# Kernel tuning notes

Hardware: AMD Instinct MI355X
Metric: run time of the kernel (lower is better)

Reference implementation:

```python
import jax, jax.numpy as jnp
import numpy as np

L, D, T, B = 4, 256, 4096, 8  # n_layer, hidden, seq_len, batch


def setup_inputs() -> dict:
    key = jax.random.key(0)
    ks = jax.random.split(key, 12)
    x = jax.random.normal(ks[0], (B, T, D), dtype=jnp.float32)
    # stable LRU diagonal init: |lambda| in [0.9, 0.999], phase in [0, pi/10]
    r = jax.random.uniform(ks[1], (L, D), minval=0.9, maxval=0.999)
    nu_log = jnp.log(-jnp.log(r))
    theta = jax.random.uniform(ks[2], (L, D), minval=1e-4, maxval=np.pi / 10)
    theta_log = jnp.log(theta)
    gamma_log = 0.5 * jnp.log(1.0 - r ** 2)  # normalization gamma = sqrt(1-|lam|^2)
    s = 0.02  # matches truncated_normal_init std
    B_re = s * jax.random.normal(ks[3], (L, D, D), dtype=jnp.float32)
    B_im = s * jax.random.normal(ks[4], (L, D, D), dtype=jnp.float32)
    C_re = s * jax.random.normal(ks[5], (L, D, D), dtype=jnp.float32)
    C_im = s * jax.random.normal(ks[6], (L, D, D), dtype=jnp.float32)
    D_vec = s * jax.random.normal(ks[7], (L, D), dtype=jnp.float32)
    Wg = s * jax.random.normal(ks[8], (L, D, D), dtype=jnp.float32)
    ln_scale = jnp.ones((L, D), dtype=jnp.float32)
    ln_bias = jnp.zeros((L, D), dtype=jnp.float32)
    return dict(x=x, nu_log=nu_log, theta_log=theta_log, gamma_log=gamma_log,
                B_re=B_re, B_im=B_im, C_re=C_re, C_im=C_im, D_vec=D_vec,
                Wg=Wg, ln_scale=ln_scale, ln_bias=ln_bias)


def _layer_norm(x, scale, bias):
    mu = x.mean(-1, keepdims=True)
    var = x.var(-1, keepdims=True)
    return (x - mu) / jnp.sqrt(var + 1e-5) * scale + bias


def _lru_scan(lam, bu):
    # lam: (D,) complex diagonal transition; bu: (T,B,D) complex inputs
    a = jnp.broadcast_to(lam, bu.shape)

    def comb(e1, e2):
        a1, b1 = e1
        a2, b2 = e2
        return a1 * a2, a2 * b1 + b2

    _, h = jax.lax.associative_scan(comb, (a, bu), axis=0)
    return h  # (T,B,D) complex


def reference(x, nu_log, theta_log, gamma_log, B_re, B_im, C_re, C_im, D_vec, Wg, ln_scale, ln_bias):
    u = jnp.transpose(x, (1, 0, 2))  # time-major (T,B,D), mirrors torch permute(1,0,2)
    for l in range(L):  # fixed small layer loop
        z = _layer_norm(u, ln_scale[l], ln_bias[l])
        lam = jnp.exp(-jnp.exp(nu_log[l]) + 1j * jnp.exp(theta_log[l]))  # (D,)
        Bm = B_re[l] + 1j * B_im[l]
        bu = jnp.einsum('tbd,ed->tbe', z.astype(jnp.complex64), Bm) * jnp.exp(gamma_log[l])
        h = _lru_scan(lam, bu)  # (T,B,D) complex state (h0 = 0, matching get_zero_internal_state)
        y = jnp.einsum('tbe,de->tbd', h, C_re[l] + 1j * C_im[l]).real + D_vec[l] * z
        y = y * jax.nn.sigmoid(jnp.einsum('tbd,ed->tbe', z, Wg[l]))  # gating=True output gate
        u = u + y  # residual
    return jnp.transpose(u, (1, 0, 2))  # back to (B,T,D)
```

## Files before the change

kernel.cpp:

```cpp
#include <hip/hip_runtime.h>
#include <hip/hip_bf16.h>

#define NLAYER 4
#define DDIM 256
#define TSEQ 4096
#define NBATCH 8
#define MROWS (NBATCH * TSEQ)
#define CLEN 32
#define NCHUNK (TSEQ / CLEN)

typedef float f32x4 __attribute__((ext_vector_type(4)));
typedef short bf16x8 __attribute__((ext_vector_type(8)));

__device__ __forceinline__ float bf2f(unsigned short u) {
    union { unsigned int i; float f; } v; v.i = ((unsigned int)u) << 16; return v.f;
}
__device__ __forceinline__ unsigned short f2bf(float f) {
    union { float f; unsigned int i; } v; v.f = f;
    unsigned int r = v.i + 0x7fffu + ((v.i >> 16) & 1u);
    return (unsigned short)(r >> 16);
}

__device__ __forceinline__ void gload16(const unsigned short* g, unsigned short* l) {
    __builtin_amdgcn_global_load_lds(
        (const __attribute__((address_space(1))) unsigned int*)g,
        (__attribute__((address_space(3))) unsigned int*)l, 16, 0, 0);
}

__global__ __launch_bounds__(256) void prepack_kernel(
    const float* __restrict__ nu_log, const float* __restrict__ theta_log,
    const float* __restrict__ gamma_log,
    const float* __restrict__ B_re, const float* __restrict__ B_im,
    const float* __restrict__ C_re, const float* __restrict__ C_im,
    const float* __restrict__ Wg,
    unsigned short* __restrict__ wBre, unsigned short* __restrict__ wBim,
    unsigned short* __restrict__ wWg, unsigned short* __restrict__ wCre,
    unsigned short* __restrict__ wCimn,
    float* __restrict__ lam_re, float* __restrict__ lam_im,
    float* __restrict__ lamC_re, float* __restrict__ lamC_im)
{
    int idx = blockIdx.x * 256 + threadIdx.x;
    const int total = NLAYER * DDIM * DDIM;
    if (idx < total) {
        int l = idx >> 16;
        int e = (idx >> 8) & 255;
        float gam = expf(gamma_log[l * DDIM + e]);
        wBre[idx]  = f2bf(B_re[idx] * gam);
        wBim[idx]  = f2bf(B_im[idx] * gam);
        wWg[idx]   = f2bf(Wg[idx]);
        wCre[idx]  = f2bf(C_re[idx]);
        wCimn[idx] = f2bf(-C_im[idx]);
    }
    if (idx < NLAYER * DDIM) {
        float mag = expf(-expf(nu_log[idx]));
        float th  = expf(theta_log[idx]);
        float ar = mag * cosf(th);
        float ai = mag * sinf(th);
        lam_re[idx] = ar;
        lam_im[idx] = ai;
        #pragma unroll
        for (int s = 0; s < 5; ++s) {
            float nr = ar * ar - ai * ai;
            float ni = 2.0f * ar * ai;
            ar = nr; ai = ni;
        }
        lamC_re[idx] = ar;
        lamC_im[idx] = ai;
    }
}

__global__ __launch_bounds__(256) void ln_kernel(
    const float* __restrict__ u, unsigned short* __restrict__ z,
    const float* __restrict__ scale, const float* __restrict__ bias,
    float2* __restrict__ rowStats)
{
    int wid = threadIdx.x >> 6;
    int lane = threadIdx.x & 63;
    int row = blockIdx.x * 4 + wid;
    const float4 v = *reinterpret_cast<const float4*>(u + (size_t)row * DDIM + lane * 4);
    float s  = v.x + v.y + v.z + v.w;
    float s2 = v.x * v.x + v.y * v.y + v.z * v.z + v.w * v.w;
    #pragma unroll
    for (int off = 32; off > 0; off >>= 1) {
        s  += __shfl_xor(s, off);
        s2 += __shfl_xor(s2, off);
    }
    float mu  = s * (1.0f / DDIM);
    float var = s2 * (1.0f / DDIM) - mu * mu;
    float inv = rsqrtf(var + 1e-5f);
    if (lane == 0) { float2 st; st.x = mu; st.y = inv; rowStats[row] = st; }
    float zv[4] = { v.x, v.y, v.z, v.w };
    ushort4 o;
    unsigned short* op = (unsigned short*)&o;
    #pragma unroll
    for (int j = 0; j < 4; ++j) {
        int d = lane * 4 + j;
        op[j] = f2bf((zv[j] - mu) * inv * scale[d] + bias[d]);
    }
    *reinterpret_cast<ushort4*>(z + (size_t)row * DDIM + lane * 4) = o;
}

__global__ __launch_bounds__(256) void gemm1_kernel(
    const unsigned short* __restrict__ z,
    const unsigned short* __restrict__ wBre, const unsigned short* __restrict__ wBim,
    const unsigned short* __restrict__ wWg,
    unsigned short* __restrict__ bure, unsigned short* __restrict__ buim,
    unsigned short* __restrict__ sg,
    const float* __restrict__ lam_re, const float* __restrict__ lam_im,
    float2* __restrict__ fin)
{
    const int m0 = blockIdx.x * 128;
    const int n0 = blockIdx.y * 64;

    __shared__ unsigned short Al[128 * 64];
    __shared__ unsigned short Wl[3][64 * 64];

    const int tid = threadIdx.x;
    const int lane = tid & 63;
    const int wid = tid >> 6;
    const int wr = wid >> 1, wc = wid & 1;
    const int lr = lane >> 3;
    const int lc = lane & 7;

    f32x4 acc[3][4][2] = {};

    for (int ko = 0; ko < 256; ko += 64) {
        #pragma unroll
        for (int it = 0; it < 4; ++it) {
            int s = wid * 4 + it;
            int r = s * 8 + lr;
            int gc = lc ^ (r & 7);
            gload16(z + (size_t)(m0 + r) * 256 + ko + gc * 8, &Al[s * 512]);
        }
        #pragma unroll
        for (int it = 0; it < 2; ++it) {
            int s = wid * 2 + it;
            int r = s * 8 + lr;
            int gc = lc ^ (r & 7);
            size_t off = (size_t)(n0 + r) * 256 + ko + gc * 8;
            gload16(wBre + off, &Wl[0][s * 512]);
            gload16(wBim + off, &Wl[1][s * 512]);
            gload16(wWg  + off, &Wl[2][s * 512]);
        }
        __syncthreads();

        #pragma unroll
        for (int k2 = 0; k2 < 64; k2 += 32) {
            int ac = (k2 >> 3) + (lane >> 4);
            bf16x8 a[4];
            #pragma unroll
            for (int mi = 0; mi < 4; ++mi) {
                int ar = wr * 64 + mi * 16 + (lane & 15);
                a[mi] = *reinterpret_cast<const bf16x8*>(&Al[ar * 64 + ((ac ^ (ar & 7)) * 8)]);
            }
            int br0 = wc * 32 + (lane & 15);
            int br1 = br0 + 16;
            #pragma unroll
            for (int mat = 0; mat < 3; ++mat) {
                bf16x8 b0 = *reinterpret_cast<const bf16x8*>(&Wl[mat][br0 * 64 + ((ac ^ (br0 & 7)) * 8)]);
                bf16x8 b1 = *reinterpret_cast<const bf16x8*>(&Wl[mat][br1 * 64 + ((ac ^ (br1 & 7)) * 8)]);
                #pragma unroll
                for (int mi = 0; mi < 4; ++mi) {
                    acc[mat][mi][0] = __builtin_amdgcn_mfma_f32_16x16x32_bf16(a[mi], b0, acc[mat][mi][0], 0, 0, 0);
                    acc[mat][mi][1] = __builtin_amdgcn_mfma_f32_16x16x32_bf16(a[mi], b1, acc[mat][mi][1], 0, 0, 0);
                }
            }
        }
        __syncthreads();
    }

    unsigned short* Tre = Al;
    unsigned short* Tim = &Wl[0][0];
    #pragma unroll
    for (int mat = 0; mat < 3; ++mat) {
        unsigned short* out = (mat == 0) ? bure : ((mat == 1) ? buim : sg);
        #pragma unroll
        for (int mi = 0; mi < 4; ++mi) {
            #pragma unroll
            for (int ni = 0; ni < 2; ++ni) {
                int cl = wc * 32 + ni * 16 + (lane & 15);
                int rl = wr * 64 + mi * 16 + (lane >> 4) * 4;
                #pragma unroll
                for (int j = 0; j < 4; ++j) {
                    float v = acc[mat][mi][ni][j];
                    unsigned short bv;
                    if (mat == 2) { bv = f2bf(1.0f / (1.0f + expf(-v))); }
                    else          { bv = f2bf(v); }
                    out[(size_t)(m0 + rl + j) * 256 + n0 + cl] = bv;
                    if (mat == 0) Tre[(rl + j) * 64 + cl] = bv;
                    if (mat == 1) Tim[(rl + j) * 64 + cl] = bv;
                }
            }
        }
    }
    __syncthreads();
    {
        const int c = tid >> 6;
        const int col = tid & 63;
        const int dglob = n0 + col;
        const float lr_ = lam_re[dglob], li_ = lam_im[dglob];
        float hr = 0.0f, hi = 0.0f;
        #pragma unroll 8
        for (int k = 0; k < CLEN; ++k) {
            int row = c * 32 + k;
            float br = bf2f(Tre[row * 64 + col]);
            float bi = bf2f(Tim[row * 64 + col]);
            float nr = fmaf(lr_, hr, fmaf(-li_, hi, br));
            float ni = fmaf(lr_, hi, fmaf(li_, hr, bi));
            hr = nr; hi = ni;
        }
        const int b = m0 >> 12;
        const int cglob = ((m0 & 4095) >> 5) + c;
        float2 o; o.x = hr; o.y = hi;
        fin[((size_t)b * 256 + dglob) * 128 + cglob] = o;
    }
}

__global__ __launch_bounds__(256) void scan_prefix_kernel(
    const float2* __restrict__ fin, float2* __restrict__ pre,
    const float* __restrict__ lamC_re, const float* __restrict__ lamC_im)
{
    const int lane = threadIdx.x & 63;
    const int w = blockIdx.x * 4 + (threadIdx.x >> 6);
    const int d = w & 255;
    const float ar = lamC_re[d], ai = lamC_im[d];
    const float4 f = *reinterpret_cast<const float4*>(fin + (size_t)w * 128 + lane * 2);
    const float f0r = f.x, f0i = f.y, f1r = f.z, f1i = f.w;
    float Tr = fmaf(ar, f0r, fmaf(-ai, f0i, f1r));
    float Ti = fmaf(ar, f0i, fmaf(ai, f0r, f1i));
    float Ar_ = ar * ar - ai * ai;
    float Ai_ = 2.0f * ar * ai;
    #pragma unroll
    for (int s = 1; s < 64; s <<= 1) {
        float ur = __shfl_up(Tr, s, 64);
        float ui = __shfl_up(Ti, s, 64);
        if (lane >= s) {
            Tr = fmaf(Ar_, ur, fmaf(-Ai_, ui, Tr));
            Ti = fmaf(Ar_, ui, fmaf(Ai_, ur, Ti));
        }
        float nr = Ar_ * Ar_ - Ai_ * Ai_;
        float ni = 2.0f * Ar_ * Ai_;
        Ar_ = nr; Ai_ = ni;
    }
    float Er = __shfl_up(Tr, 1, 64);
    float Ei = __shfl_up(Ti, 1, 64);
    if (lane == 0) { Er = 0.0f; Ei = 0.0f; }
    float P1r = fmaf(ar, Er, fmaf(-ai, Ei, f0r));
    float P1i = fmaf(ar, Ei, fmaf(ai, Er, f0i));
    float4 o; o.x = Er; o.y = Ei; o.z = P1r; o.w = P1i;
    *reinterpret_cast<float4*>(pre + (size_t)w * 128 + lane * 2) = o;
}

__global__ __launch_bounds__(256) void gemm2_kernel(
    const unsigned short* __restrict__ bure, const unsigned short* __restrict__ buim,
    const unsigned short* __restrict__ wCre, const unsigned short* __restrict__ wCimn,
    const unsigned short* __restrict__ sg, const float2* __restrict__ pre,
    const float* __restrict__ lam_re, const float* __restrict__ lam_im,
    const float* __restrict__ scale, const float* __restrict__ bias,
    const float2* __restrict__ rowStats,
    const float* __restrict__ Dv, const float* __restrict__ uin, float* __restrict__ uout,
    const float* __restrict__ nscale, const float* __restrict__ nbias,
    unsigned short* __restrict__ zout, float2* __restrict__ statsOut, int writeLN)
{
    const int m0 = blockIdx.x * 64;

    __shared__ unsigned short Ar[64 * 64];
    __shared__ unsigned short Ai[64 * 64];
    __shared__ unsigned short Cr[256 * 64];
    __shared__ unsigned short Ci[256 * 64];

    const int tid = threadIdx.x;
    const int lane = tid & 63;
    const int wid = tid >> 6;
    const int lr = lane >> 3;
    const int lc = lane & 7;

    const int b = m0 >> 12;
    const int cbase = (m0 & 4095) >> 5;

    f32x4 acc[4][4] = {};

    for (int ko = 0; ko < 256; ko += 64) {
        #pragma unroll
        for (int it = 0; it < 2; ++it) {
            int s = wid * 2 + it;
            int r = s * 8 + lr;
            int gc = lc ^ (r & 7);
            size_t off = (size_t)(m0 + r) * 256 + ko + gc * 8;
            gload16(bure + off, &Ar[s * 512]);
            gload16(buim + off, &Ai[s * 512]);
        }
        #pragma unroll
        for (int it = 0; it < 8; ++it) {
            int s = wid * 8 + it;
            int r = s * 8 + lr;
            int gc = lc ^ (r & 7);
            size_t off = (size_t)r * 256 + ko + gc * 8;
            gload16(wCre + off, &Cr[s * 512]);
            gload16(wCimn + off, &Ci[s * 512]);
        }
        __syncthreads();

        if (tid < 128) {
            const int c = tid >> 6;
            const int dl = tid & 63;
            const int dg = ko + dl;
            const float lre = lam_re[dg], lim = lam_im[dg];
            float2 p = pre[((size_t)b * 256 + dg) * 128 + cbase + c];
            float hr = p.x, hi = p.y;
            #pragma unroll 8
            for (int k = 0; k < CLEN; ++k) {
                int row = c * 32 + k;
                int off = row * 64 + (((dl >> 3) ^ (row & 7)) * 8) + (dl & 7);
                float br = bf2f(Ar[off]);
                float bi = bf2f(Ai[off]);
                float nr = fmaf(lre, hr, fmaf(-lim, hi, br));
                float ni = fmaf(lre, hi, fmaf(lim, hr, bi));
                hr = nr; hi = ni;
                Ar[off] = f2bf(nr);
                Ai[off] = f2bf(ni);
            }
        }
        __syncthreads();

        #pragma unroll
        for (int k2 = 0; k2 < 64; k2 += 32) {
            int ac = (k2 >> 3) + (lane >> 4);
            bf16x8 are[4], aim[4];
            #pragma unroll
            for (int mi = 0; mi < 4; ++mi) {
                int arow = mi * 16 + (lane & 15);
                int idx = arow * 64 + ((ac ^ (arow & 7)) * 8);
                are[mi] = *reinterpret_cast<const bf16x8*>(&Ar[idx]);
                aim[mi] = *reinterpret_cast<const bf16x8*>(&Ai[idx]);
            }
            #pragma unroll
            for (int ni = 0; ni < 4; ++ni) {
                int brow = wid * 64 + ni * 16 + (lane & 15);
                int ib = brow * 64 + ((ac ^ (brow & 7)) * 8);
                bf16x8 bre = *reinterpret_cast<const bf16x8*>(&Cr[ib]);
                bf16x8 bim = *reinterpret_cast<const bf16x8*>(&Ci[ib]);
                #pragma unroll
                for (int mi = 0; mi < 4; ++mi) {
                    acc[mi][ni] = __builtin_amdgcn_mfma_f32_16x16x32_bf16(are[mi], bre, acc[mi][ni], 0, 0, 0);
                    acc[mi][ni] = __builtin_amdgcn_mfma_f32_16x16x32_bf16(aim[mi], bim, acc[mi][ni], 0, 0, 0);
                }
            }
        }
        __syncthreads();
    }

    float uvals[4][4][4];
    float rs[4][4], rs2[4][4];
    #pragma unroll
    for (int mi = 0; mi < 4; ++mi)
        #pragma unroll
        for (int j = 0; j < 4; ++j) { rs[mi][j] = 0.0f; rs2[mi][j] = 0.0f; }

    #pragma unroll
    for (int mi = 0; mi < 4; ++mi) {
        #pragma unroll
        for (int ni = 0; ni < 4; ++ni) {
            int col = wid * 64 + ni * 16 + (lane & 15);
            int mrow = m0 + mi * 16 + (lane >> 4) * 4;
            float dv = Dv[col];
            float scc = scale[col], bcc = bias[col];
            #pragma unroll
            for (int j = 0; j < 4; ++j) {
                size_t idx = (size_t)(mrow + j) * 256 + col;
                float2 st = rowStats[mrow + j];
                float uv = uin[idx];
                float zz = (uv - st.x) * st.y * scc + bcc;
                float s = bf2f(sg[idx]);
                float o = uv + (acc[mi][ni][j] + dv * zz) * s;
                uout[idx] = o;
                uvals[mi][ni][j] = o;
                rs[mi][j] += o;
                rs2[mi][j] += o * o;
            }
        }
    }

    if (writeLN) {
        #pragma unroll
        for (int mi = 0; mi < 4; ++mi)
            #pragma unroll
            for (int j = 0; j < 4; ++j)
                #pragma unroll
                for (int off = 1; off < 16; off <<= 1) {
                    rs[mi][j]  += __shfl_xor(rs[mi][j], off);
                    rs2[mi][j] += __shfl_xor(rs2[mi][j], off);
                }
        float* sS   = (float*)Ar;
        float* sS2  = sS + 256;
        float* sMu  = sS2 + 256;
        float* sInv = sMu + 64;
        __syncthreads();
        if ((lane & 15) == 0) {
            int hi = lane >> 4;
            #pragma unroll
            for (int mi = 0; mi < 4; ++mi)
                #pragma unroll
                for (int j = 0; j < 4; ++j) {
                    int row = mi * 16 + hi * 4 + j;
                    sS[wid * 64 + row]  = rs[mi][j];
                    sS2[wid * 64 + row] = rs2[mi][j];
                }
        }
        __syncthreads();
        if (tid < 64) {
            float s  = sS[tid] + sS[64 + tid] + sS[128 + tid] + sS[192 + tid];
            float s2 = sS2[tid] + sS2[64 + tid] + sS2[128 + tid] + sS2[192 + tid];
            float mu  = s * (1.0f / 256.0f);
            float var = s2 * (1.0f / 256.0f) - mu * mu;
            float inv = rsqrtf(var + 1e-5f);
            sMu[tid] = mu; sInv[tid] = inv;
            float2 st; st.x = mu; st.y = inv;
            statsOut[m0 + tid] = st;
        }
        __syncthreads();
        #pragma unroll
        for (int mi = 0; mi < 4; ++mi) {
            #pragma unroll
            for (int ni = 0; ni < 4; ++ni) {
                int col = wid * 64 + ni * 16 + (lane & 15);
                float nsc = nscale[col], nbi = nbias[col];
                #pragma unroll
                for (int j = 0; j < 4; ++j) {
                    int row = mi * 16 + (lane >> 4) * 4 + j;
                    float zz = (uvals[mi][ni][j] - sMu[row]) * sInv[row] * nsc + nbi;
                    zout[(size_t)(m0 + row) * 256 + col] = f2bf(zz);
                }
            }
        }
    }
}

extern "C" void kernel_launch(void* const* d_in, const int* in_sizes, int n_in,
                              void* d_out, int out_size, void* d_ws, size_t ws_size,
                              hipStream_t stream) {
    const float* x         = (const float*)d_in[0];
    const float* nu_log    = (const float*)d_in[1];
    const float* theta_log = (const float*)d_in[2];
    const float* gamma_log = (const float*)d_in[3];
    const float* B_re      = (const float*)d_in[4];
    const float* B_im      = (const float*)d_in[5];
    const float* C_re      = (const float*)d_in[6];
    const float* C_im      = (const float*)d_in[7];
    const float* D_vec     = (const float*)d_in[8];
    const float* Wg        = (const float*)d_in[9];
    const float* ln_scale  = (const float*)d_in[10];
    const float* ln_bias   = (const float*)d_in[11];
    float* out = (float*)d_out;

    const size_t MSZ = (size_t)MROWS * DDIM;
    const size_t WSZ = (size_t)NLAYER * DDIM * DDIM;
    const size_t FSZ = (size_t)NBATCH * DDIM * NCHUNK;

    unsigned short* b16 = (unsigned short*)d_ws;
    unsigned short* z     = b16;
    unsigned short* sg    = b16 + MSZ;
    unsigned short* bure  = b16 + 2 * MSZ;
    unsigned short* buim  = b16 + 3 * MSZ;
    unsigned short* wBre  = b16 + 4 * MSZ;
    unsigned short* wBim  = wBre + WSZ;
    unsigned short* wWg   = wBim + WSZ;
    unsigned short* wCre  = wWg + WSZ;
    unsigned short* wCimn = wCre + WSZ;
    float* lam_re  = (float*)(wCimn + WSZ);
    float* lam_im  = lam_re + NLAYER * DDIM;
    float* lamC_re = lam_im + NLAYER * DDIM;
    float* lamC_im = lamC_re + NLAYER * DDIM;
    float2* fin = (float2*)(lamC_im + NLAYER * DDIM);
    float2* pre = fin + FSZ;
    float2* statsA = pre + FSZ;
    float2* statsB = statsA + MROWS;

    prepack_kernel<<<1024, 256, 0, stream>>>(nu_log, theta_log, gamma_log,
                                             B_re, B_im, C_re, C_im, Wg,
                                             wBre, wBim, wWg, wCre, wCimn,
                                             lam_re, lam_im, lamC_re, lamC_im);

    ln_kernel<<<MROWS / 4, 256, 0, stream>>>(x, z, ln_scale, ln_bias, statsA);

    for (int l = 0; l < NLAYER; ++l) {
        const float* uin = (l == 0) ? x : out;
        const float* lre = lam_re + l * DDIM;
        const float* lim = lam_im + l * DDIM;
        float2* statsIn  = (l & 1) ? statsB : statsA;
        float2* statsOut = (l & 1) ? statsA : statsB;
        int nl = (l < NLAYER - 1) ? (l + 1) : l;
        gemm1_kernel<<<dim3(MROWS / 128, 4), 256, 0, stream>>>(
            z, wBre + l * DDIM * DDIM, wBim + l * DDIM * DDIM, wWg + l * DDIM * DDIM,
            bure, buim, sg, lre, lim, fin);
        scan_prefix_kernel<<<512, 256, 0, stream>>>(fin, pre,
                                                    lamC_re + l * DDIM, lamC_im + l * DDIM);
        gemm2_kernel<<<MROWS / 64, 256, 0, stream>>>(
            bure, buim, wCre + l * DDIM * DDIM, wCimn + l * DDIM * DDIM,
            sg, pre, lre, lim,
            ln_scale + l * DDIM, ln_bias + l * DDIM, statsIn,
            D_vec + l * DDIM, uin, out,
            ln_scale + nl * DDIM, ln_bias + nl * DDIM,
            z, statsOut, (l < NLAYER - 1) ? 1 : 0);
    }
}
```

Baseline: 287.5 us.

## Store chunk-local scan states in gemm1 and apply prefix correction in gemm2

gemm1 now writes the chunk-local recurrence states (h with zero initial state) to global memory instead of raw bu, and the scan in gemm2 becomes a parallel additive correction: each element gets the carried prefix times a power of lambda. This lets all 256 threads work in gemm2's scan phase, using lambda^16 to split each chunk into two halves, rather than 128 threads running a serial 32-step dependent recurrence. The cost is a strided per-step global store pattern in gemm1's scan loop and an extra bf16 rounding on the stored states.

```diff
diff --git a/kernel.cpp b/kernel.cpp
--- a/kernel.cpp
+++ b/kernel.cpp
@@ -37,6 +37,7 @@
     unsigned short* __restrict__ wWg, unsigned short* __restrict__ wCre,
     unsigned short* __restrict__ wCimn,
     float* __restrict__ lam_re, float* __restrict__ lam_im,
+    float* __restrict__ lamH_re, float* __restrict__ lamH_im,
     float* __restrict__ lamC_re, float* __restrict__ lamC_im)
 {
     int idx = blockIdx.x * 256 + threadIdx.x;
@@ -59,13 +60,19 @@
         lam_re[idx] = ar;
         lam_im[idx] = ai;
         #pragma unroll
-        for (int s = 0; s < 5; ++s) {
+        for (int s = 0; s < 4; ++s) {
             float nr = ar * ar - ai * ai;
             float ni = 2.0f * ar * ai;
             ar = nr; ai = ni;
         }
-        lamC_re[idx] = ar;
-        lamC_im[idx] = ai;
+        lamH_re[idx] = ar;
+        lamH_im[idx] = ai;
+        {
+            float nr = ar * ar - ai * ai;
+            float ni = 2.0f * ar * ai;
+            lamC_re[idx] = nr;
+            lamC_im[idx] = ni;
+        }
     }
 }
 
@@ -104,7 +111,7 @@
     const unsigned short* __restrict__ z,
     const unsigned short* __restrict__ wBre, const unsigned short* __restrict__ wBim,
     const unsigned short* __restrict__ wWg,
-    unsigned short* __restrict__ bure, unsigned short* __restrict__ buim,
+    unsigned short* __restrict__ hlre, unsigned short* __restrict__ hlim,
     unsigned short* __restrict__ sg,
     const float* __restrict__ lam_re, const float* __restrict__ lam_im,
     float2* __restrict__ fin)
@@ -172,24 +179,17 @@
     unsigned short* Tre = Al;
     unsigned short* Tim = &Wl[0][0];
     #pragma unroll
-    for (int mat = 0; mat < 3; ++mat) {
-        unsigned short* out = (mat == 0) ? bure : ((mat == 1) ? buim : sg);
-        #pragma unroll
-        for (int mi = 0; mi < 4; ++mi) {
-            #pragma unroll
-            for (int ni = 0; ni < 2; ++ni) {
-                int cl = wc * 32 + ni * 16 + (lane & 15);
-                int rl = wr * 64 + mi * 16 + (lane >> 4) * 4;
-                #pragma unroll
-                for (int j = 0; j < 4; ++j) {
-                    float v = acc[mat][mi][ni][j];
-                    unsigned short bv;
-                    if (mat == 2) { bv = f2bf(1.0f / (1.0f + expf(-v))); }
-                    else          { bv = f2bf(v); }
-                    out[(size_t)(m0 + rl + j) * 256 + n0 + cl] = bv;
-                    if (mat == 0) Tre[(rl + j) * 64 + cl] = bv;
-                    if (mat == 1) Tim[(rl + j) * 64 + cl] = bv;
-                }
+    for (int mi = 0; mi < 4; ++mi) {
+        #pragma unroll
+        for (int ni = 0; ni < 2; ++ni) {
+            int cl = wc * 32 + ni * 16 + (lane & 15);
+            int rl = wr * 64 + mi * 16 + (lane >> 4) * 4;
+            #pragma unroll
+            for (int j = 0; j < 4; ++j) {
+                Tre[(rl + j) * 64 + cl] = f2bf(acc[0][mi][ni][j]);
+                Tim[(rl + j) * 64 + cl] = f2bf(acc[1][mi][ni][j]);
+                float g = acc[2][mi][ni][j];
+                sg[(size_t)(m0 + rl + j) * 256 + n0 + cl] = f2bf(1.0f / (1.0f + expf(-g)));
             }
         }
     }
@@ -200,6 +200,7 @@
         const int dglob = n0 + col;
         const float lr_ = lam_re[dglob], li_ = lam_im[dglob];
         float hr = 0.0f, hi = 0.0f;
+        size_t gbase = (size_t)(m0 + c * 32) * 256 + dglob;
         #pragma unroll 8
         for (int k = 0; k < CLEN; ++k) {
             int row = c * 32 + k;
@@ -208,6 +209,8 @@
             float nr = fmaf(lr_, hr, fmaf(-li_, hi, br));
             float ni = fmaf(lr_, hi, fmaf(li_, hr, bi));
             hr = nr; hi = ni;
+            hlre[gbase + (size_t)k * 256] = f2bf(hr);
+            hlim[gbase + (size_t)k * 256] = f2bf(hi);
         }
         const int b = m0 >> 12;
         const int cglob = ((m0 & 4095) >> 5) + c;
@@ -252,10 +255,11 @@
 }
 
 __global__ __launch_bounds__(256) void gemm2_kernel(
-    const unsigned short* __restrict__ bure, const unsigned short* __restrict__ buim,
+    const unsigned short* __restrict__ hlre, const unsigned short* __restrict__ hlim,
     const unsigned short* __restrict__ wCre, const unsigned short* __restrict__ wCimn,
     const unsigned short* __restrict__ sg, const float2* __restrict__ pre,
     const float* __restrict__ lam_re, const float* __restrict__ lam_im,
+    const float* __restrict__ lamH_re, const float* __restrict__ lamH_im,
     const float* __restrict__ scale, const float* __restrict__ bias,
     const float2* __restrict__ rowStats,
     const float* __restrict__ Dv, const float* __restrict__ uin, float* __restrict__ uout,
@@ -278,6 +282,15 @@
     const int b = m0 >> 12;
     const int cbase = (m0 & 4095) >> 5;
 
+    const int cdl   = tid & 63;
+    const int chalf = (tid >> 6) & 1;
+    const int cch   = tid >> 7;
+
+    float2 pre4[4];
+    #pragma unroll
+    for (int kk = 0; kk < 4; ++kk)
+        pre4[kk] = pre[((size_t)b * 256 + kk * 64 + cdl) * 128 + cbase + cch];
+
     f32x4 acc[4][4] = {};
 
     for (int ko = 0; ko < 256; ko += 64) {
@@ -287,8 +300,8 @@
             int r = s * 8 + lr;
             int gc = lc ^ (r & 7);
             size_t off = (size_t)(m0 + r) * 256 + ko + gc * 8;
-            gload16(bure + off, &Ar[s * 512]);
-            gload16(buim + off, &Ai[s * 512]);
+            gload16(hlre + off, &Ar[s * 512]);
+            gload16(hlim + off, &Ai[s * 512]);
         }
         #pragma unroll
         for (int it = 0; it < 8; ++it) {
@@ -301,24 +314,29 @@
         }
         __syncthreads();
 
-        if (tid < 128) {
-            const int c = tid >> 6;
-            const int dl = tid & 63;
-            const int dg = ko + dl;
+        {
+            const int dg = ko + cdl;
             const float lre = lam_re[dg], lim = lam_im[dg];
-            float2 p = pre[((size_t)b * 256 + dg) * 128 + cbase + c];
-            float hr = p.x, hi = p.y;
-            #pragma unroll 8
-            for (int k = 0; k < CLEN; ++k) {
-                int row = c * 32 + k;
-                int off = row * 64 + (((dl >> 3) ^ (row & 7)) * 8) + (dl & 7);
-                float br = bf2f(Ar[off]);
-                float bi = bf2f(Ai[off]);
-                float nr = fmaf(lre, hr, fmaf(-lim, hi, br));
-                float ni = fmaf(lre, hi, fmaf(lim, hr, bi));
-                hr = nr; hi = ni;
-                Ar[off] = f2bf(nr);
-                Ai[off] = f2bf(ni);
+            float qr, qi;
+            if (chalf == 0) { qr = lre; qi = lim; }
+            else {
+                float hre16 = lamH_re[dg], him16 = lamH_im[dg];
+                qr = hre16 * lre - him16 * lim;
+                qi = hre16 * lim + him16 * lre;
+            }
+            const int kk = ko >> 6;
+            float Pr = pre4[kk].x, Pi = pre4[kk].y;
+            float tr = qr * Pr - qi * Pi;
+            float ti = qr * Pi + qi * Pr;
+            #pragma unroll
+            for (int k = 0; k < 16; ++k) {
+                int row = cch * 32 + chalf * 16 + k;
+                int off = row * 64 + (((cdl >> 3) ^ (row & 7)) * 8) + (cdl & 7);
+                Ar[off] = f2bf(bf2f(Ar[off]) + tr);
+                Ai[off] = f2bf(bf2f(Ai[off]) + ti);
+                float ntr = lre * tr - lim * ti;
+                float nti = lre * ti + lim * tr;
+                tr = ntr; ti = nti;
             }
         }
         __syncthreads();
@@ -460,8 +478,8 @@
     unsigned short* b16 = (unsigned short*)d_ws;
     unsigned short* z     = b16;
     unsigned short* sg    = b16 + MSZ;
-    unsigned short* bure  = b16 + 2 * MSZ;
-    unsigned short* buim  = b16 + 3 * MSZ;
+    unsigned short* hlre  = b16 + 2 * MSZ;
+    unsigned short* hlim  = b16 + 3 * MSZ;
     unsigned short* wBre  = b16 + 4 * MSZ;
     unsigned short* wBim  = wBre + WSZ;
     unsigned short* wWg   = wBim + WSZ;
@@ -469,7 +487,9 @@
     unsigned short* wCimn = wCre + WSZ;
     float* lam_re  = (float*)(wCimn + WSZ);
     float* lam_im  = lam_re + NLAYER * DDIM;
-    float* lamC_re = lam_im + NLAYER * DDIM;
+    float* lamH_re = lam_im + NLAYER * DDIM;
+    float* lamH_im = lamH_re + NLAYER * DDIM;
+    float* lamC_re = lamH_im + NLAYER * DDIM;
     float* lamC_im = lamC_re + NLAYER * DDIM;
     float2* fin = (float2*)(lamC_im + NLAYER * DDIM);
     float2* pre = fin + FSZ;
@@ -479,7 +499,8 @@
     prepack_kernel<<<1024, 256, 0, stream>>>(nu_log, theta_log, gamma_log,
                                              B_re, B_im, C_re, C_im, Wg,
                                              wBre, wBim, wWg, wCre, wCimn,
-                                             lam_re, lam_im, lamC_re, lamC_im);
+                                             lam_re, lam_im, lamH_re, lamH_im,
+                                             lamC_re, lamC_im);
 
     ln_kernel<<<MROWS / 4, 256, 0, stream>>>(x, z, ln_scale, ln_bias, statsA);
 
@@ -492,12 +513,12 @@
         int nl = (l < NLAYER - 1) ? (l + 1) : l;
         gemm1_kernel<<<dim3(MROWS / 128, 4), 256, 0, stream>>>(
             z, wBre + l * DDIM * DDIM, wBim + l * DDIM * DDIM, wWg + l * DDIM * DDIM,
-            bure, buim, sg, lre, lim, fin);
+            hlre, hlim, sg, lre, lim, fin);
         scan_prefix_kernel<<<512, 256, 0, stream>>>(fin, pre,
                                                     lamC_re + l * DDIM, lamC_im + l * DDIM);
         gemm2_kernel<<<MROWS / 64, 256, 0, stream>>>(
-            bure, buim, wCre + l * DDIM * DDIM, wCimn + l * DDIM * DDIM,
-            sg, pre, lre, lim,
+            hlre, hlim, wCre + l * DDIM * DDIM, wCimn + l * DDIM * DDIM,
+            sg, pre, lre, lim, lamH_re + l * DDIM, lamH_im + l * DDIM,
             ln_scale + l * DDIM, ln_bias + l * DDIM, statsIn,
             D_vec + l * DDIM, uin, out,
             ln_scale + nl * DDIM, ln_bias + nl * DDIM,
```

After: 363.2 us. 26.4% more time.
